# Optimization experiments

Hardware: AMD Instinct MI355X
Metric: run time of the kernel (lower is better)

## Reference

```python
import jax, jax.numpy as jnp
import numpy as np

B, DIM = 16384, 1024
H1, H2, H3 = 500, 200, 200


def setup_inputs() -> dict:
    key = jax.random.key(0)
    ks = jax.random.split(key, 16)
    s = 0.01
    return {
        "x": jax.random.normal(ks[0], (B, DIM), dtype=jnp.float32),
        "show_index": jax.random.randint(ks[1], (B,), 0, 100),
        "st": jax.random.normal(ks[2], (1000, 16), dtype=jnp.float32),
        # deep MLP params (shared across the two task heads, as in the source)
        "W1": jax.random.normal(ks[3], (DIM, H1), dtype=jnp.float32) * s,
        "b1": jnp.zeros((H1,), dtype=jnp.float32),
        "W2": jax.random.normal(ks[4], (H1, H2), dtype=jnp.float32) * s,
        "b2": jnp.zeros((H2,), dtype=jnp.float32),
        "W3": jax.random.normal(ks[5], (H2, H3), dtype=jnp.float32) * s,
        "b3": jnp.zeros((H3,), dtype=jnp.float32),
        # final sigmoid head on concat([emb(DIM), d3(H3)])
        "Wl": jax.random.normal(ks[6], (DIM + H3, 1), dtype=jnp.float32) * s,
        "bl": jnp.zeros((1,), dtype=jnp.float32),
        # per-(task, cross-layer) cross weights/biases: tf.random_normal stddev=0.01
        "cw": jax.random.normal(ks[7], (2, 3, DIM), dtype=jnp.float32) * s,
        "cb": jax.random.normal(ks[8], (2, 3, DIM), dtype=jnp.float32) * s,
    }


def reference(x, show_index, st, W1, b1, W2, b2, W3, b3, Wl, bl, cw, cb):
    # Deep part (same shared Dense layers each task -> compute once).
    d = jax.nn.relu(x @ W1 + b1)
    d = jax.nn.relu(d @ W2 + b2)
    d3 = jax.nn.relu(d @ W3 + b3)  # (B, H3)

    # cross_net: sum_i w[j] * x[b,i] * emb[b,j]  ==  x.sum(1) * emb[b,j] * w[j]
    # (collapsed form of the (B,dim,dim) outer product + axis-1 reduction)
    xsum = jnp.sum(x, axis=1, keepdims=True)  # (B, 1)
    preds = []
    for i in range(2):
        emb = x
        for j in range(3):
            emb = xsum * emb * cw[i, j] + cb[i, j] + x
        mid = jnp.concatenate([emb, d3], axis=-1)  # (B, DIM+H3)
        preds.append(jax.nn.sigmoid(mid @ Wl + bl))  # (B, 1)
    return tuple(preds)
```

## Files before the change

kernel.cpp:

```cpp
#include <hip/hip_runtime.h>
#include <hip/hip_bf16.h>
#include <math.h>

#define B_ROWS 16384
#define DIM 1024

typedef __attribute__((ext_vector_type(8))) short s16x8;
typedef __attribute__((ext_vector_type(4))) float f32x4;

static __device__ __forceinline__ unsigned short f2bf(float f) {
    union { float f; unsigned u; } v; v.f = f;
    unsigned r = v.u + 0x7FFF + ((v.u >> 16) & 1);
    return (unsigned short)(r >> 16);
}

static __device__ __forceinline__ void gload16(const unsigned short* g, unsigned short* l) {
    __builtin_amdgcn_global_load_lds(
        (const __attribute__((address_space(1))) unsigned int*)g,
        (__attribute__((address_space(3))) unsigned int*)l, 16, 0, 0);
}

__global__ __launch_bounds__(256) void prep(
    const float* __restrict__ x, unsigned short* __restrict__ xb,
    const float* __restrict__ W1, const float* __restrict__ W2,
    const float* __restrict__ W3,
    const float* __restrict__ cw, const float* __restrict__ cb,
    const float* __restrict__ Wl,
    unsigned short* __restrict__ W1b, unsigned short* __restrict__ W2b,
    unsigned short* __restrict__ W3b,
    float* __restrict__ czz) {
    __shared__ unsigned short tile[64][72];
    __shared__ float red[4][6];
    const int tid = threadIdx.x;
    const int blk = blockIdx.x;

    if (blk < 4096) {
        const float* src = x + (size_t)blk * 4096;
        unsigned short* dst = xb + (size_t)blk * 4096;
#pragma unroll
        for (int r = 0; r < 4; ++r) {
            float4 f = *(const float4*)(src + r * 1024 + tid * 4);
            short4 h;
            h.x = (short)f2bf(f.x); h.y = (short)f2bf(f.y);
            h.z = (short)f2bf(f.z); h.w = (short)f2bf(f.w);
            *(short4*)(dst + r * 1024 + tid * 4) = h;
        }
    } else if (blk < 4272) {
        const int w = blk - 4096;
        const float* src; unsigned short* dst;
        int kt, nt, Ksrc, Nsrc, ldDst;
        bool skipHi = false;
        if (w < 128)      { kt = w & 15;         nt = w >> 4;         src = W1; dst = W1b; Ksrc = 1024; Nsrc = 500; ldDst = 1024; skipHi = true; }
        else if (w < 160) { kt = (w - 128) & 7;  nt = (w - 128) >> 3; src = W2; dst = W2b; Ksrc = 500;  Nsrc = 200; ldDst = 512;  }
        else              { kt = (w - 160) & 3;  nt = (w - 160) >> 2; src = W3; dst = W3b; Ksrc = 200;  Nsrc = 200; ldDst = 256;  }
        const int k0 = kt << 6, n0 = nt << 6;
        {
            const int r = tid >> 2, c0 = (tid & 3) << 4;
            const int kk = k0 + r;
#pragma unroll
            for (int i = 0; i < 16; ++i) {
                const int nn = n0 + c0 + i;
                const float v = (kk < Ksrc && nn < Nsrc) ? src[(size_t)kk * Nsrc + nn] : 0.f;
                tile[r][c0 + i] = f2bf(v);
            }
        }
        __syncthreads();
        {
            const int n = tid >> 2, kc = (tid & 3) << 4;
            if (!(skipHi && (n0 + n) >= 500)) {
                unsigned short* o = dst + (size_t)(n0 + n) * ldDst + k0 + kc;
#pragma unroll
                for (int i = 0; i < 16; ++i) o[i] = tile[kc + i][n];
            }
        }
    } else if (blk == 4272) {
#pragma unroll
        for (int q = 0; q < 4; ++q) {
            const int k = tid * 4 + q;
            const float wl = Wl[k];
            const float a1 = cw[k],        a2 = cw[1024 + k], a3 = cw[2048 + k];
            const float d1_ = cw[3072 + k], d2_ = cw[4096 + k], d3_ = cw[5120 + k];
            W1b[(size_t)500 * 1024 + k] = f2bf(a1 * a2 * a3 * wl);
            W1b[(size_t)501 * 1024 + k] = f2bf(a2 * a3 * wl);
            W1b[(size_t)502 * 1024 + k] = f2bf(a3 * wl);
            W1b[(size_t)503 * 1024 + k] = f2bf(d1_ * d2_ * d3_ * wl);
            W1b[(size_t)504 * 1024 + k] = f2bf(d2_ * d3_ * wl);
            W1b[(size_t)505 * 1024 + k] = f2bf(d3_ * wl);
            W1b[(size_t)506 * 1024 + k] = f2bf(wl);
            W1b[(size_t)507 * 1024 + k] = 0x3F80;
            W1b[(size_t)508 * 1024 + k] = 0;
            W1b[(size_t)509 * 1024 + k] = 0;
            W1b[(size_t)510 * 1024 + k] = 0;
            W1b[(size_t)511 * 1024 + k] = 0;
        }
    } else {
        float c[6] = {0.f, 0.f, 0.f, 0.f, 0.f, 0.f};
#pragma unroll
        for (int q = 0; q < 4; ++q) {
            const int k = tid * 4 + q;
            const float wl = Wl[k];
            {
                const float w2 = cw[1024 + k], w3 = cw[2048 + k];
                const float b1 = cb[k], b2 = cb[1024 + k], b3 = cb[2048 + k];
                c[0] += w2 * w3 * b1 * wl;
                c[1] += w3 * b2 * wl;
                c[2] += b3 * wl;
            }
            {
                const float w2 = cw[4096 + k], w3 = cw[5120 + k];
                const float b1 = cb[3072 + k], b2 = cb[4096 + k], b3 = cb[5120 + k];
                c[3] += w2 * w3 * b1 * wl;
                c[4] += w3 * b2 * wl;
                c[5] += b3 * wl;
            }
        }
        const int lane = tid & 63, wv = tid >> 6;
#pragma unroll
        for (int j = 0; j < 6; ++j)
#pragma unroll
            for (int m = 1; m < 64; m <<= 1) c[j] += __shfl_xor(c[j], m, 64);
        if (lane == 0)
#pragma unroll
            for (int j = 0; j < 6; ++j) red[wv][j] = c[j];
        __syncthreads();
        if (tid < 6) czz[tid] = red[0][tid] + red[1][tid] + red[2][tid] + red[3][tid];
    }
}

template <int ROWS>
static __device__ __forceinline__ void stage_tile(
    const unsigned short* __restrict__ src, int K, int rowBase, int kt,
    unsigned short* lds, int w, int lane) {
    const int r8   = lane >> 3;
    const int slot = lane & 7;
#pragma unroll
    for (int q = 0; q < ROWS / 32; ++q) {
        const int blk   = q * 4 + w;
        const int row   = blk * 8 + r8;
        const int chunk = slot ^ (row & 7);
        const unsigned short* g = src + (size_t)(rowBase + row) * K + kt * 64 + chunk * 8;
        gload16(g, lds + blk * 512);
    }
}

template <int BM>
__global__ __launch_bounds__(256) void gemm_bf16(
    const unsigned short* __restrict__ A,
    const unsigned short* __restrict__ Bw,
    const float* __restrict__ bias, int biasN,
    unsigned short* __restrict__ C,
    float* __restrict__ zparts,
    int K, int ldc) {
    constexpr int MREP = BM / 32;
    __shared__ unsigned short As[2][BM * 64];
    __shared__ unsigned short Bs[2][128 * 64];

    const int tid  = threadIdx.x;
    const int lane = tid & 63;
    const int wid  = tid >> 6;
    const int wm   = wid >> 1;
    const int wn   = wid & 1;
    const int g    = lane >> 4;
    const int r16  = lane & 15;

    const int cpx = gridDim.x >> 3;
    const int swz = (blockIdx.x & 7) * cpx + (blockIdx.x >> 3);
    const int nColTiles = ldc >> 7;
    const int rowBase = (swz / nColTiles) * BM;
    const int colBase = (swz % nColTiles) << 7;

    f32x4 acc[MREP][4];
#pragma unroll
    for (int m = 0; m < MREP; ++m)
#pragma unroll
        for (int n = 0; n < 4; ++n)
            acc[m][n] = (f32x4){0.f, 0.f, 0.f, 0.f};

    stage_tile<BM>(A, K, rowBase, 0, As[0], wid, lane);
    stage_tile<128>(Bw, K, colBase, 0, Bs[0], wid, lane);

    const int nK = K >> 6;
    for (int kt = 0; kt < nK; ++kt) {
        const int buf = kt & 1;
        if (kt + 1 < nK) {
            stage_tile<BM>(A, K, rowBase, kt + 1, As[buf ^ 1], wid, lane);
            stage_tile<128>(Bw, K, colBase, kt + 1, Bs[buf ^ 1], wid, lane);
            if constexpr (BM == 128)
                asm volatile("s_waitcnt vmcnt(8)" ::: "memory");
            else
                asm volatile("s_waitcnt vmcnt(6)" ::: "memory");
        } else {
            asm volatile("s_waitcnt vmcnt(0)" ::: "memory");
        }
        __builtin_amdgcn_s_barrier();
        asm volatile("" ::: "memory");

        const unsigned short* Ab = As[buf];
        const unsigned short* Bb = Bs[buf];
#pragma unroll
        for (int ks = 0; ks < 2; ++ks) {
            s16x8 af[MREP], bfr[4];
#pragma unroll
            for (int m = 0; m < MREP; ++m) {
                const int row = wm * (BM / 2) + m * 16 + r16;
                const int off = ((ks * 4 + g) * 16) ^ ((row & 7) << 4);
                af[m] = *(const s16x8*)((const char*)Ab + row * 128 + off);
            }
#pragma unroll
            for (int n = 0; n < 4; ++n) {
                const int row = wn * 64 + n * 16 + r16;
                const int off = ((ks * 4 + g) * 16) ^ ((row & 7) << 4);
                bfr[n] = *(const s16x8*)((const char*)Bb + row * 128 + off);
            }
#pragma unroll
            for (int m = 0; m < MREP; ++m)
#pragma unroll
                for (int n = 0; n < 4; ++n)
                    acc[m][n] = __builtin_amdgcn_mfma_f32_16x16x32_bf16(af[m], bfr[n], acc[m][n], 0, 0, 0);
        }
        asm volatile("s_waitcnt lgkmcnt(0)" ::: "memory");
        __builtin_amdgcn_s_barrier();
        asm volatile("" ::: "memory");
    }

#pragma unroll
    for (int n = 0; n < 4; ++n) {
        const int col = colBase + wn * 64 + n * 16 + r16;
        const float bv = (col < biasN) ? bias[col] : 0.f;
        const unsigned pc = (unsigned)(col - 500);
#pragma unroll
        for (int m = 0; m < MREP; ++m) {
            const int rowB = rowBase + wm * (BM / 2) + m * 16 + g * 4;
#pragma unroll
            for (int r = 0; r < 4; ++r) {
                const float raw = acc[m][n][r];
                float v = raw + bv;
                v = v > 0.f ? v : 0.f;
                C[(size_t)(rowB + r) * ldc + col] = f2bf(v);
                if (pc < 8u) zparts[(size_t)(rowB + r) * 8 + pc] = raw;
            }
        }
    }
}

__global__ __launch_bounds__(256) void tail_fused(
    const unsigned short* __restrict__ d1,
    const unsigned short* __restrict__ W2b,
    const float* __restrict__ b2,
    const unsigned short* __restrict__ W3b,
    const float* __restrict__ b3,
    const float* __restrict__ Wl,
    const float* __restrict__ bl,
    const float* __restrict__ zparts,
    const float* __restrict__ czz,
    float* __restrict__ out) {
    __shared__ unsigned short As[2][64 * 64];
    __shared__ unsigned short Bs[2][256 * 64];
    __shared__ unsigned short P[64 * 256];
    __shared__ float part[4][64];

    const int tid  = threadIdx.x;
    const int lane = tid & 63;
    const int wid  = tid >> 6;
    const int g    = lane >> 4;
    const int r16  = lane & 15;
    const int rowBase = blockIdx.x << 6;

    f32x4 acc[4][4];
#pragma unroll
    for (int m = 0; m < 4; ++m)
#pragma unroll
        for (int n = 0; n < 4; ++n)
            acc[m][n] = (f32x4){0.f, 0.f, 0.f, 0.f};

    stage_tile<64>(d1, 512, rowBase, 0, As[0], wid, lane);
    stage_tile<256>(W2b, 512, 0, 0, Bs[0], wid, lane);

    for (int kt = 0; kt < 8; ++kt) {
        const int buf = kt & 1;
        if (kt + 1 < 8) {
            stage_tile<64>(d1, 512, rowBase, kt + 1, As[buf ^ 1], wid, lane);
            stage_tile<256>(W2b, 512, 0, kt + 1, Bs[buf ^ 1], wid, lane);
            asm volatile("s_waitcnt vmcnt(10)" ::: "memory");
        } else {
            asm volatile("s_waitcnt vmcnt(0)" ::: "memory");
        }
        __builtin_amdgcn_s_barrier();
        asm volatile("" ::: "memory");

        const unsigned short* Ab = As[buf];
        const unsigned short* Bb = Bs[buf];
#pragma unroll
        for (int ks = 0; ks < 2; ++ks) {
            s16x8 af[4], bfr[4];
#pragma unroll
            for (int m = 0; m < 4; ++m) {
                const int row = m * 16 + r16;
                const int off = ((ks * 4 + g) * 16) ^ ((row & 7) << 4);
                af[m] = *(const s16x8*)((const char*)Ab + row * 128 + off);
            }
#pragma unroll
            for (int n = 0; n < 4; ++n) {
                const int row = wid * 64 + n * 16 + r16;
                const int off = ((ks * 4 + g) * 16) ^ ((row & 7) << 4);
                bfr[n] = *(const s16x8*)((const char*)Bb + row * 128 + off);
            }
#pragma unroll
            for (int m = 0; m < 4; ++m)
#pragma unroll
                for (int n = 0; n < 4; ++n)
                    acc[m][n] = __builtin_amdgcn_mfma_f32_16x16x32_bf16(af[m], bfr[n], acc[m][n], 0, 0, 0);
        }
        asm volatile("s_waitcnt lgkmcnt(0)" ::: "memory");
        __builtin_amdgcn_s_barrier();
        asm volatile("" ::: "memory");
    }

#pragma unroll
    for (int n = 0; n < 4; ++n) {
        const int col = wid * 64 + n * 16 + r16;
        const float bv = (col < 200) ? b2[col] : 0.f;
#pragma unroll
        for (int m = 0; m < 4; ++m) {
#pragma unroll
            for (int r = 0; r < 4; ++r) {
                const int row = m * 16 + g * 4 + r;
                float v = acc[m][n][r] + bv;
                v = v > 0.f ? v : 0.f;
                const int byte = row * 512 + ((col * 2) ^ ((row & 7) << 4));
                *(unsigned short*)((char*)P + byte) = f2bf(v);
            }
        }
    }

    stage_tile<256>(W3b, 256, 0, 0, Bs[0], wid, lane);
    asm volatile("s_waitcnt lgkmcnt(0)" ::: "memory");
    __builtin_amdgcn_s_barrier();
    asm volatile("" ::: "memory");

    f32x4 acc2[4][4];
#pragma unroll
    for (int m = 0; m < 4; ++m)
#pragma unroll
        for (int n = 0; n < 4; ++n)
            acc2[m][n] = (f32x4){0.f, 0.f, 0.f, 0.f};

    for (int kt = 0; kt < 4; ++kt) {
        const int buf = kt & 1;
        if (kt + 1 < 4) {
            stage_tile<256>(W3b, 256, 0, kt + 1, Bs[buf ^ 1], wid, lane);
            asm volatile("s_waitcnt vmcnt(8)" ::: "memory");
        } else {
            asm volatile("s_waitcnt vmcnt(0)" ::: "memory");
        }
        __builtin_amdgcn_s_barrier();
        asm volatile("" ::: "memory");

        const unsigned short* Bb = Bs[buf];
#pragma unroll
        for (int ks = 0; ks < 2; ++ks) {
            s16x8 af[4], bfr[4];
#pragma unroll
            for (int m = 0; m < 4; ++m) {
                const int row = m * 16 + r16;
                const int byte = row * 512 + ((kt * 128 + (ks * 4 + g) * 16) ^ ((row & 7) << 4));
                af[m] = *(const s16x8*)((const char*)P + byte);
            }
#pragma unroll
            for (int n = 0; n < 4; ++n) {
                const int row = wid * 64 + n * 16 + r16;
                const int off = ((ks * 4 + g) * 16) ^ ((row & 7) << 4);
                bfr[n] = *(const s16x8*)((const char*)Bb + row * 128 + off);
            }
#pragma unroll
            for (int m = 0; m < 4; ++m)
#pragma unroll
                for (int n = 0; n < 4; ++n)
                    acc2[m][n] = __builtin_amdgcn_mfma_f32_16x16x32_bf16(af[m], bfr[n], acc2[m][n], 0, 0, 0);
        }
        asm volatile("s_waitcnt lgkmcnt(0)" ::: "memory");
        __builtin_amdgcn_s_barrier();
        asm volatile("" ::: "memory");
    }

    float wlv[4], b3v[4];
#pragma unroll
    for (int n = 0; n < 4; ++n) {
        const int col = wid * 64 + n * 16 + r16;
        wlv[n] = (col < 200) ? Wl[1024 + col] : 0.f;
        b3v[n] = (col < 200) ? b3[col] : 0.f;
    }
#pragma unroll
    for (int m = 0; m < 4; ++m) {
#pragma unroll
        for (int r = 0; r < 4; ++r) {
            float s = 0.f;
#pragma unroll
            for (int n = 0; n < 4; ++n) {
                float v = acc2[m][n][r] + b3v[n];
                v = v > 0.f ? v : 0.f;
                s += v * wlv[n];
            }
            s += __shfl_xor(s, 1, 64);
            s += __shfl_xor(s, 2, 64);
            s += __shfl_xor(s, 4, 64);
            s += __shfl_xor(s, 8, 64);
            if (r16 == 0) part[wid][m * 16 + g * 4 + r] = s;
        }
    }
    __syncthreads();

    if (tid < 64) {
        const int row = rowBase + tid;
        const float t = part[0][tid] + part[1][tid] + part[2][tid] + part[3][tid];
        const float blv = bl[0];
        const float* zp = zparts + (size_t)row * 8;
        float4 zpa = *(const float4*)(zp);
        float4 zpb = *(const float4*)(zp + 4);
        const float s = zpb.w;
        const float z0 = ((zpa.x * s + zpa.y + czz[0]) * s + zpa.z + czz[1]) * s
                         + zpb.z + czz[2] + t + blv;
        const float z1 = ((zpa.w * s + zpb.x + czz[3]) * s + zpb.y + czz[4]) * s
                         + zpb.z + czz[5] + t + blv;
        out[row]          = 1.f / (1.f + expf(-z0));
        out[B_ROWS + row] = 1.f / (1.f + expf(-z1));
    }
}

extern "C" void kernel_launch(void* const* d_in, const int* in_sizes, int n_in,
                              void* d_out, int out_size, void* d_ws, size_t ws_size,
                              hipStream_t stream) {
    const float* x  = (const float*)d_in[0];
    const float* W1 = (const float*)d_in[3];
    const float* b1 = (const float*)d_in[4];
    const float* W2 = (const float*)d_in[5];
    const float* b2 = (const float*)d_in[6];
    const float* W3 = (const float*)d_in[7];
    const float* b3 = (const float*)d_in[8];
    const float* Wl = (const float*)d_in[9];
    const float* bl = (const float*)d_in[10];
    const float* cw = (const float*)d_in[11];
    const float* cb = (const float*)d_in[12];
    float* out = (float*)d_out;

    unsigned short* xb  = (unsigned short*)d_ws;
    unsigned short* d1  = xb + (size_t)16384 * 1024;
    unsigned short* W1b = d1 + (size_t)16384 * 512;
    unsigned short* W2b = W1b + (size_t)512 * 1024;
    unsigned short* W3b = W2b + (size_t)256 * 512;
    float* zparts = (float*)(W3b + (size_t)256 * 256);
    float* czz = zparts + (size_t)16384 * 8;

    prep<<<4274, 256, 0, stream>>>(x, xb, W1, W2, W3, cw, cb, Wl,
                                   W1b, W2b, W3b, czz);

    gemm_bf16<128><<<512, 256, 0, stream>>>(xb, W1b, b1, 500, d1, zparts, 1024, 512);

    tail_fused<<<256, 256, 0, stream>>>(d1, W2b, b2, W3b, b3, Wl, bl,
                                        zparts, czz, out);
}
```

Measured before the change: 64.34 us.

## Fuse fp32-to-bf16 conversion of x into first GEMM and widen tail kernel

The prep pass that converted all of x to bf16 in a workspace buffer is removed. The first GEMM now loads fp32 x rows into registers, converts them with packed bf16 conversion instructions and writes them swizzled into LDS, prefetching one k-tile ahead. This drops a full write and re-read of the 32 MB bf16 copy of x. Separately, the tail kernel moves to 512 threads with a 2x4 wave layout, which halves per-wave accumulator work and may improve latency hiding, at the cost of more register pressure and synchronisation per block.

```diff
diff --git a/kernel.cpp b/kernel.cpp
--- a/kernel.cpp
+++ b/kernel.cpp
@@ -14,6 +14,12 @@
     return (unsigned short)(r >> 16);
 }
 
+static __device__ __forceinline__ unsigned cvt_pk_bf16(float lo, float hi) {
+    unsigned r;
+    asm volatile("v_cvt_pk_bf16_f32 %0, %1, %2" : "=v"(r) : "v"(lo), "v"(hi));
+    return r;
+}
+
 static __device__ __forceinline__ void gload16(const unsigned short* g, unsigned short* l) {
     __builtin_amdgcn_global_load_lds(
         (const __attribute__((address_space(1))) unsigned int*)g,
@@ -21,7 +27,6 @@
 }
 
 __global__ __launch_bounds__(256) void prep(
-    const float* __restrict__ x, unsigned short* __restrict__ xb,
     const float* __restrict__ W1, const float* __restrict__ W2,
     const float* __restrict__ W3,
     const float* __restrict__ cw, const float* __restrict__ cb,
@@ -34,19 +39,8 @@
     const int tid = threadIdx.x;
     const int blk = blockIdx.x;
 
-    if (blk < 4096) {
-        const float* src = x + (size_t)blk * 4096;
-        unsigned short* dst = xb + (size_t)blk * 4096;
-#pragma unroll
-        for (int r = 0; r < 4; ++r) {
-            float4 f = *(const float4*)(src + r * 1024 + tid * 4);
-            short4 h;
-            h.x = (short)f2bf(f.x); h.y = (short)f2bf(f.y);
-            h.z = (short)f2bf(f.z); h.w = (short)f2bf(f.w);
-            *(short4*)(dst + r * 1024 + tid * 4) = h;
-        }
-    } else if (blk < 4272) {
-        const int w = blk - 4096;
+    if (blk < 176) {
+        const int w = blk;
         const float* src; unsigned short* dst;
         int kt, nt, Ksrc, Nsrc, ldDst;
         bool skipHi = false;
@@ -73,12 +67,12 @@
                 for (int i = 0; i < 16; ++i) o[i] = tile[kc + i][n];
             }
         }
-    } else if (blk == 4272) {
+    } else if (blk == 176) {
 #pragma unroll
         for (int q = 0; q < 4; ++q) {
             const int k = tid * 4 + q;
             const float wl = Wl[k];
-            const float a1 = cw[k],        a2 = cw[1024 + k], a3 = cw[2048 + k];
+            const float a1 = cw[k],         a2 = cw[1024 + k],  a3 = cw[2048 + k];
             const float d1_ = cw[3072 + k], d2_ = cw[4096 + k], d3_ = cw[5120 + k];
             W1b[(size_t)500 * 1024 + k] = f2bf(a1 * a2 * a3 * wl);
             W1b[(size_t)501 * 1024 + k] = f2bf(a2 * a3 * wl);
@@ -143,15 +137,29 @@
     }
 }
 
-template <int BM>
-__global__ __launch_bounds__(256) void gemm_bf16(
-    const unsigned short* __restrict__ A,
+template <int ROWS>
+static __device__ __forceinline__ void stage8(
+    const unsigned short* __restrict__ src, int K, int rowBase, int kt,
+    unsigned short* lds, int w, int lane) {
+    const int r8   = lane >> 3;
+    const int slot = lane & 7;
+#pragma unroll
+    for (int q = 0; q < ROWS / 64; ++q) {
+        const int blk   = q * 8 + w;
+        const int row   = blk * 8 + r8;
+        const int chunk = slot ^ (row & 7);
+        const unsigned short* g = src + (size_t)(rowBase + row) * K + kt * 64 + chunk * 8;
+        gload16(g, lds + blk * 512);
+    }
+}
+
+__global__ __launch_bounds__(256) void gemm_xa(
+    const float* __restrict__ X,
     const unsigned short* __restrict__ Bw,
-    const float* __restrict__ bias, int biasN,
+    const float* __restrict__ bias,
     unsigned short* __restrict__ C,
-    float* __restrict__ zparts,
-    int K, int ldc) {
-    constexpr int MREP = BM / 32;
+    float* __restrict__ zparts) {
+    constexpr int K = 1024, ldc = 512, BM = 128, nK = 16;
     __shared__ unsigned short As[2][BM * 64];
     __shared__ unsigned short Bs[2][128 * 64];
 
@@ -165,44 +173,69 @@
 
     const int cpx = gridDim.x >> 3;
     const int swz = (blockIdx.x & 7) * cpx + (blockIdx.x >> 3);
-    const int nColTiles = ldc >> 7;
-    const int rowBase = (swz / nColTiles) * BM;
-    const int colBase = (swz % nColTiles) << 7;
-
-    f32x4 acc[MREP][4];
-#pragma unroll
-    for (int m = 0; m < MREP; ++m)
+    const int rowBase = (swz >> 2) * BM;
+    const int colBase = (swz & 3) << 7;
+
+    const int arow  = tid >> 1;
+    const int ahalf = tid & 1;
+    const float* aSrc = X + (size_t)(rowBase + arow) * K + ahalf * 32;
+    const int arw = arow & 7;
+
+    float4 a_regs[8];
+
+    f32x4 acc[4][4];
+#pragma unroll
+    for (int m = 0; m < 4; ++m)
 #pragma unroll
         for (int n = 0; n < 4; ++n)
             acc[m][n] = (f32x4){0.f, 0.f, 0.f, 0.f};
 
-    stage_tile<BM>(A, K, rowBase, 0, As[0], wid, lane);
+    {
+        const float* s = aSrc;
+#pragma unroll
+        for (int i = 0; i < 8; ++i) a_regs[i] = *(const float4*)(s + i * 4);
+    }
+    asm volatile("" ::: "memory");
     stage_tile<128>(Bw, K, colBase, 0, Bs[0], wid, lane);
-
-    const int nK = K >> 6;
+    asm volatile("" ::: "memory");
+    {
+#pragma unroll
+        for (int j = 0; j < 4; ++j) {
+            uint4 v;
+            v.x = cvt_pk_bf16(a_regs[2 * j].x, a_regs[2 * j].y);
+            v.y = cvt_pk_bf16(a_regs[2 * j].z, a_regs[2 * j].w);
+            v.z = cvt_pk_bf16(a_regs[2 * j + 1].x, a_regs[2 * j + 1].y);
+            v.w = cvt_pk_bf16(a_regs[2 * j + 1].z, a_regs[2 * j + 1].w);
+            const int ch = (ahalf * 4 + j) ^ arw;
+            *(uint4*)((char*)As[0] + arow * 128 + ch * 16) = v;
+        }
+    }
+    asm volatile("" ::: "memory");
+    {
+        const float* s = aSrc + 64;
+#pragma unroll
+        for (int i = 0; i < 8; ++i) a_regs[i] = *(const float4*)(s + i * 4);
+    }
+    asm volatile("s_waitcnt vmcnt(8)" ::: "memory");
+    asm volatile("s_waitcnt lgkmcnt(0)" ::: "memory");
+    __builtin_amdgcn_s_barrier();
+    asm volatile("" ::: "memory");
+
     for (int kt = 0; kt < nK; ++kt) {
         const int buf = kt & 1;
         if (kt + 1 < nK) {
-            stage_tile<BM>(A, K, rowBase, kt + 1, As[buf ^ 1], wid, lane);
             stage_tile<128>(Bw, K, colBase, kt + 1, Bs[buf ^ 1], wid, lane);
-            if constexpr (BM == 128)
-                asm volatile("s_waitcnt vmcnt(8)" ::: "memory");
-            else
-                asm volatile("s_waitcnt vmcnt(6)" ::: "memory");
-        } else {
-            asm volatile("s_waitcnt vmcnt(0)" ::: "memory");
-        }
-        __builtin_amdgcn_s_barrier();
-        asm volatile("" ::: "memory");
+            asm volatile("" ::: "memory");
+        }
 
         const unsigned short* Ab = As[buf];
         const unsigned short* Bb = Bs[buf];
 #pragma unroll
         for (int ks = 0; ks < 2; ++ks) {
-            s16x8 af[MREP], bfr[4];
-#pragma unroll
-            for (int m = 0; m < MREP; ++m) {
-                const int row = wm * (BM / 2) + m * 16 + r16;
+            s16x8 af[4], bfr[4];
+#pragma unroll
+            for (int m = 0; m < 4; ++m) {
+                const int row = wm * 64 + m * 16 + r16;
                 const int off = ((ks * 4 + g) * 16) ^ ((row & 7) << 4);
                 af[m] = *(const s16x8*)((const char*)Ab + row * 128 + off);
             }
@@ -213,10 +246,34 @@
                 bfr[n] = *(const s16x8*)((const char*)Bb + row * 128 + off);
             }
 #pragma unroll
-            for (int m = 0; m < MREP; ++m)
+            for (int m = 0; m < 4; ++m)
 #pragma unroll
                 for (int n = 0; n < 4; ++n)
                     acc[m][n] = __builtin_amdgcn_mfma_f32_16x16x32_bf16(af[m], bfr[n], acc[m][n], 0, 0, 0);
+        }
+
+        if (kt + 1 < nK) {
+#pragma unroll
+            for (int j = 0; j < 4; ++j) {
+                uint4 v;
+                v.x = cvt_pk_bf16(a_regs[2 * j].x, a_regs[2 * j].y);
+                v.y = cvt_pk_bf16(a_regs[2 * j].z, a_regs[2 * j].w);
+                v.z = cvt_pk_bf16(a_regs[2 * j + 1].x, a_regs[2 * j + 1].y);
+                v.w = cvt_pk_bf16(a_regs[2 * j + 1].z, a_regs[2 * j + 1].w);
+                const int ch = (ahalf * 4 + j) ^ arw;
+                *(uint4*)((char*)As[buf ^ 1] + arow * 128 + ch * 16) = v;
+            }
+            asm volatile("" ::: "memory");
+            if (kt + 2 < nK) {
+                const float* s = aSrc + (kt + 2) * 64;
+#pragma unroll
+                for (int i = 0; i < 8; ++i) a_regs[i] = *(const float4*)(s + i * 4);
+                asm volatile("s_waitcnt vmcnt(8)" ::: "memory");
+            } else {
+                asm volatile("s_waitcnt vmcnt(0)" ::: "memory");
+            }
+        } else {
+            asm volatile("s_waitcnt vmcnt(0)" ::: "memory");
         }
         asm volatile("s_waitcnt lgkmcnt(0)" ::: "memory");
         __builtin_amdgcn_s_barrier();
@@ -226,11 +283,11 @@
 #pragma unroll
     for (int n = 0; n < 4; ++n) {
         const int col = colBase + wn * 64 + n * 16 + r16;
-        const float bv = (col < biasN) ? bias[col] : 0.f;
+        const float bv = (col < 500) ? bias[col] : 0.f;
         const unsigned pc = (unsigned)(col - 500);
 #pragma unroll
-        for (int m = 0; m < MREP; ++m) {
-            const int rowB = rowBase + wm * (BM / 2) + m * 16 + g * 4;
+        for (int m = 0; m < 4; ++m) {
+            const int rowB = rowBase + wm * 64 + m * 16 + g * 4;
 #pragma unroll
             for (int r = 0; r < 4; ++r) {
                 const float raw = acc[m][n][r];
@@ -243,7 +300,7 @@
     }
 }
 
-__global__ __launch_bounds__(256) void tail_fused(
+__global__ __launch_bounds__(512) void tail_fused(
     const unsigned short* __restrict__ d1,
     const unsigned short* __restrict__ W2b,
     const float* __restrict__ b2,
@@ -257,31 +314,33 @@
     __shared__ unsigned short As[2][64 * 64];
     __shared__ unsigned short Bs[2][256 * 64];
     __shared__ unsigned short P[64 * 256];
-    __shared__ float part[4][64];
+    __shared__ float part[8][64];
 
     const int tid  = threadIdx.x;
     const int lane = tid & 63;
     const int wid  = tid >> 6;
+    const int wm   = wid >> 2;
+    const int wn   = wid & 3;
     const int g    = lane >> 4;
     const int r16  = lane & 15;
     const int rowBase = blockIdx.x << 6;
 
-    f32x4 acc[4][4];
-#pragma unroll
-    for (int m = 0; m < 4; ++m)
+    f32x4 acc[2][4];
+#pragma unroll
+    for (int m = 0; m < 2; ++m)
 #pragma unroll
         for (int n = 0; n < 4; ++n)
             acc[m][n] = (f32x4){0.f, 0.f, 0.f, 0.f};
 
-    stage_tile<64>(d1, 512, rowBase, 0, As[0], wid, lane);
-    stage_tile<256>(W2b, 512, 0, 0, Bs[0], wid, lane);
+    stage8<64>(d1, 512, rowBase, 0, As[0], wid, lane);
+    stage8<256>(W2b, 512, 0, 0, Bs[0], wid, lane);
 
     for (int kt = 0; kt < 8; ++kt) {
         const int buf = kt & 1;
         if (kt + 1 < 8) {
-            stage_tile<64>(d1, 512, rowBase, kt + 1, As[buf ^ 1], wid, lane);
-            stage_tile<256>(W2b, 512, 0, kt + 1, Bs[buf ^ 1], wid, lane);
-            asm volatile("s_waitcnt vmcnt(10)" ::: "memory");
+            stage8<64>(d1, 512, rowBase, kt + 1, As[buf ^ 1], wid, lane);
+            stage8<256>(W2b, 512, 0, kt + 1, Bs[buf ^ 1], wid, lane);
+            asm volatile("s_waitcnt vmcnt(5)" ::: "memory");
         } else {
             asm volatile("s_waitcnt vmcnt(0)" ::: "memory");
         }
@@ -292,21 +351,21 @@
         const unsigned short* Bb = Bs[buf];
 #pragma unroll
         for (int ks = 0; ks < 2; ++ks) {
-            s16x8 af[4], bfr[4];
-#pragma unroll
-            for (int m = 0; m < 4; ++m) {
-                const int row = m * 16 + r16;
+            s16x8 af[2], bfr[4];
+#pragma unroll
+            for (int m = 0; m < 2; ++m) {
+                const int row = wm * 32 + m * 16 + r16;
                 const int off = ((ks * 4 + g) * 16) ^ ((row & 7) << 4);
                 af[m] = *(const s16x8*)((const char*)Ab + row * 128 + off);
             }
 #pragma unroll
             for (int n = 0; n < 4; ++n) {
-                const int row = wid * 64 + n * 16 + r16;
+                const int row = wn * 64 + n * 16 + r16;
                 const int off = ((ks * 4 + g) * 16) ^ ((row & 7) << 4);
                 bfr[n] = *(const s16x8*)((const char*)Bb + row * 128 + off);
             }
 #pragma unroll
-            for (int m = 0; m < 4; ++m)
+            for (int m = 0; m < 2; ++m)
 #pragma unroll
                 for (int n = 0; n < 4; ++n)
                     acc[m][n] = __builtin_amdgcn_mfma_f32_16x16x32_bf16(af[m], bfr[n], acc[m][n], 0, 0, 0);
@@ -318,13 +377,13 @@
 
 #pragma unroll
     for (int n = 0; n < 4; ++n) {
-        const int col = wid * 64 + n * 16 + r16;
+        const int col = wn * 64 + n * 16 + r16;
         const float bv = (col < 200) ? b2[col] : 0.f;
 #pragma unroll
-        for (int m = 0; m < 4; ++m) {
+        for (int m = 0; m < 2; ++m) {
 #pragma unroll
             for (int r = 0; r < 4; ++r) {
-                const int row = m * 16 + g * 4 + r;
+                const int row = wm * 32 + m * 16 + g * 4 + r;
                 float v = acc[m][n][r] + bv;
                 v = v > 0.f ? v : 0.f;
                 const int byte = row * 512 + ((col * 2) ^ ((row & 7) << 4));
@@ -333,14 +392,14 @@
         }
     }
 
-    stage_tile<256>(W3b, 256, 0, 0, Bs[0], wid, lane);
+    stage8<256>(W3b, 256, 0, 0, Bs[0], wid, lane);
     asm volatile("s_waitcnt lgkmcnt(0)" ::: "memory");
     __builtin_amdgcn_s_barrier();
     asm volatile("" ::: "memory");
 
-    f32x4 acc2[4][4];
-#pragma unroll
-    for (int m = 0; m < 4; ++m)
+    f32x4 acc2[2][4];
+#pragma unroll
+    for (int m = 0; m < 2; ++m)
 #pragma unroll
         for (int n = 0; n < 4; ++n)
             acc2[m][n] = (f32x4){0.f, 0.f, 0.f, 0.f};
@@ -348,8 +407,8 @@
     for (int kt = 0; kt < 4; ++kt) {
         const int buf = kt & 1;
         if (kt + 1 < 4) {
-            stage_tile<256>(W3b, 256, 0, kt + 1, Bs[buf ^ 1], wid, lane);
-            asm volatile("s_waitcnt vmcnt(8)" ::: "memory");
+            stage8<256>(W3b, 256, 0, kt + 1, Bs[buf ^ 1], wid, lane);
+            asm volatile("s_waitcnt vmcnt(4)" ::: "memory");
         } else {
             asm volatile("s_waitcnt vmcnt(0)" ::: "memory");
         }
@@ -359,21 +418,21 @@
         const unsigned short* Bb = Bs[buf];
 #pragma unroll
         for (int ks = 0; ks < 2; ++ks) {
-            s16x8 af[4], bfr[4];
-#pragma unroll
-            for (int m = 0; m < 4; ++m) {
-                const int row = m * 16 + r16;
+            s16x8 af[2], bfr[4];
+#pragma unroll
+            for (int m = 0; m < 2; ++m) {
+                const int row = wm * 32 + m * 16 + r16;
                 const int byte = row * 512 + ((kt * 128 + (ks * 4 + g) * 16) ^ ((row & 7) << 4));
                 af[m] = *(const s16x8*)((const char*)P + byte);
             }
 #pragma unroll
             for (int n = 0; n < 4; ++n) {
-                const int row = wid * 64 + n * 16 + r16;
+                const int row = wn * 64 + n * 16 + r16;
                 const int off = ((ks * 4 + g) * 16) ^ ((row & 7) << 4);
                 bfr[n] = *(const s16x8*)((const char*)Bb + row * 128 + off);
             }
 #pragma unroll
-            for (int m = 0; m < 4; ++m)
+            for (int m = 0; m < 2; ++m)
 #pragma unroll
                 for (int n = 0; n < 4; ++n)
                     acc2[m][n] = __builtin_amdgcn_mfma_f32_16x16x32_bf16(af[m], bfr[n], acc2[m][n], 0, 0, 0);
@@ -386,12 +445,12 @@
     float wlv[4], b3v[4];
 #pragma unroll
     for (int n = 0; n < 4; ++n) {
-        const int col = wid * 64 + n * 16 + r16;
+        const int col = wn * 64 + n * 16 + r16;
         wlv[n] = (col < 200) ? Wl[1024 + col] : 0.f;
         b3v[n] = (col < 200) ? b3[col] : 0.f;
     }
 #pragma unroll
-    for (int m = 0; m < 4; ++m) {
+    for (int m = 0; m < 2; ++m) {
 #pragma unroll
         for (int r = 0; r < 4; ++r) {
             float s = 0.f;
@@ -405,14 +464,16 @@
             s += __shfl_xor(s, 2, 64);
             s += __shfl_xor(s, 4, 64);
             s += __shfl_xor(s, 8, 64);
-            if (r16 == 0) part[wid][m * 16 + g * 4 + r] = s;
+            if (r16 == 0) part[wid][wm * 32 + m * 16 + g * 4 + r] = s;
         }
     }
     __syncthreads();
 
     if (tid < 64) {
         const int row = rowBase + tid;
-        const float t = part[0][tid] + part[1][tid] + part[2][tid] + part[3][tid];
+        const int wmr = (tid >> 5) << 2;
+        const float t = part[wmr][tid] + part[wmr + 1][tid] +
+                        part[wmr + 2][tid] + part[wmr + 3][tid];
         const float blv = bl[0];
         const float* zp = zparts + (size_t)row * 8;
         float4 zpa = *(const float4*)(zp);
@@ -443,19 +504,17 @@
     const float* cb = (const float*)d_in[12];
     float* out = (float*)d_out;
 
-    unsigned short* xb  = (unsigned short*)d_ws;
-    unsigned short* d1  = xb + (size_t)16384 * 1024;
+    unsigned short* d1  = (unsigned short*)d_ws;
     unsigned short* W1b = d1 + (size_t)16384 * 512;
     unsigned short* W2b = W1b + (size_t)512 * 1024;
     unsigned short* W3b = W2b + (size_t)256 * 512;
     float* zparts = (float*)(W3b + (size_t)256 * 256);
     float* czz = zparts + (size_t)16384 * 8;
 
-    prep<<<4274, 256, 0, stream>>>(x, xb, W1, W2, W3, cw, cb, Wl,
-                                   W1b, W2b, W3b, czz);
-
-    gemm_bf16<128><<<512, 256, 0, stream>>>(xb, W1b, b1, 500, d1, zparts, 1024, 512);
-
-    tail_fused<<<256, 256, 0, stream>>>(d1, W2b, b2, W3b, b3, Wl, bl,
+    prep<<<178, 256, 0, stream>>>(W1, W2, W3, cw, cb, Wl, W1b, W2b, W3b, czz);
+
+    gemm_xa<<<512, 256, 0, stream>>>(x, W1b, b1, d1, zparts);
+
+    tail_fused<<<256, 512, 0, stream>>>(d1, W2b, b2, W3b, b3, Wl, bl,
                                         zparts, czz, out);
 }
```

Measured after the change: 66.98 us. 1.04x slower.
